# Performance work log

Hardware: AMD Instinct MI355X
Metric: run time of the kernel (lower is better)

The kernel has to match this reference:

```python
import jax, jax.numpy as jnp
import numpy as np

N_NODES = 100000
N_EDGES = 1600000
N_FEAT = 128
N_HID = 128


def cheb_conv_k2(x, edge_index, W0, W1, b):
    """PyG ChebConv with K=2, sym norm, lambda_max=2.0.
    Reduces to: out = x @ W0 + (L_hat x) @ W1 + b, where
    L_hat = 2L/lambda_max - I = -D^{-1/2} A D^{-1/2} (diagonal cancels).
    """
    n = x.shape[0]
    row, col = edge_index[0], edge_index[1]
    deg = jax.ops.segment_sum(jnp.ones_like(row, dtype=x.dtype), row, num_segments=n)
    dinv = jnp.where(deg > 0, jax.lax.rsqrt(jnp.maximum(deg, 1.0)), 0.0)
    w = -(dinv[row] * dinv[col])                     # [E] edge weights of L_hat
    tx1 = jax.ops.segment_sum(x[col] * w[:, None], row, num_segments=n)  # [N, F]
    return x @ W0 + tx1 @ W1 + b


def setup_inputs() -> dict:
    key = jax.random.key(0)
    ks = jax.random.split(key, 8)
    glorot = lambda k, fi, fo: jax.random.normal(k, (fi, fo), dtype=jnp.float32) * np.float32(np.sqrt(2.0 / (fi + fo)))
    x = jax.random.normal(ks[0], (N_NODES, N_FEAT), dtype=jnp.float32)
    edge_index = jax.random.randint(ks[1], (2, N_EDGES), 0, N_NODES, dtype=jnp.int64 if jax.config.jax_enable_x64 else jnp.int32)
    return {
        "x": x,
        "edge_index": edge_index,
        "W0_1": glorot(ks[2], N_FEAT, N_HID),
        "W1_1": glorot(ks[3], N_FEAT, N_HID),
        "b1": jnp.zeros((N_HID,), dtype=jnp.float32),
        "W0_2": glorot(ks[4], N_HID, N_HID),
        "W1_2": glorot(ks[5], N_HID, N_HID),
        "b2": jnp.zeros((N_HID,), dtype=jnp.float32),
    }


def reference(x, edge_index, W0_1, W1_1, b1, W0_2, W1_2, b2):
    # eval mode: input Dropout, dropout_adj(p=0.8), and per-layer Dropout are identity
    x1 = jax.nn.relu(cheb_conv_k2(x, edge_index, W0_1, W1_1, b1))
    x2 = jax.nn.relu(cheb_conv_k2(x1, edge_index, W0_2, W1_2, b2))
    # mean of the two layer outputs; outAct is identity
    return (x1 + x2) * 0.5
```

## Files before the change

kernel.cpp:

```cpp
#include <hip/hip_runtime.h>

#define NN 100000
#define NE 1600000
#define NF 128
#define NSTRIP2 (NN / 32)
#define NBUCK ((NN + 127) / 128)
#define CAP 2560
#define CHUNK 8192

typedef __attribute__((ext_vector_type(8))) short short8;
typedef __attribute__((ext_vector_type(4))) float f32x4;

__device__ __forceinline__ unsigned short f2b(float f) {
    union { float f; unsigned int u; } v; v.f = f;
    unsigned int u = v.u;
    unsigned int r = (u + 0x7fffu + ((u >> 16) & 1u)) >> 16;
    return (unsigned short)r;
}
__device__ __forceinline__ unsigned int cvtpk(float lo, float hi) {
    unsigned int r;
    asm("v_cvt_pk_bf16_f32 %0, %1, %2" : "=v"(r) : "v"(lo), "v"(hi));
    return r;
}

__global__ __launch_bounds__(512) void k_bin(const int* __restrict__ row,
                                             const int* __restrict__ col,
                                             int* __restrict__ gcur,
                                             unsigned int* __restrict__ gslab) {
    __shared__ int hist[NBUCK];
    __shared__ int start[NBUCK];
    __shared__ int gbase[NBUCK];
    __shared__ int scanbuf[512];
    __shared__ unsigned int stage[CHUNK];
    __shared__ unsigned short sb[CHUNK];

    const int t = threadIdx.x;
    const int e0 = blockIdx.x * CHUNK;
    const int cnt = min(CHUNK, NE - e0);

    for (int i = t; i < NBUCK; i += 512) hist[i] = 0;
    __syncthreads();
    for (int i = t; i < cnt; i += 512) atomicAdd(&hist[row[e0 + i] >> 7], 1);
    __syncthreads();

    const int b0 = t * 2;
    int s = 0;
#pragma unroll
    for (int k = 0; k < 2; ++k) { int idx = b0 + k; if (idx < NBUCK) s += hist[idx]; }
    scanbuf[t] = s;
    __syncthreads();
    for (int off = 1; off < 512; off <<= 1) {
        int u = t >= off ? scanbuf[t - off] : 0;
        __syncthreads();
        scanbuf[t] += u;
        __syncthreads();
    }
    int run = t > 0 ? scanbuf[t - 1] : 0;
#pragma unroll
    for (int k = 0; k < 2; ++k) {
        int idx = b0 + k;
        if (idx < NBUCK) { start[idx] = run; run += hist[idx]; }
    }
    __syncthreads();

    for (int i = t; i < NBUCK; i += 512) {
        int c = hist[i];
        gbase[i] = c > 0 ? atomicAdd(&gcur[i], c) : 0;
        hist[i] = start[i];
    }
    __syncthreads();

    for (int i = t; i < cnt; i += 512) {
        int r = row[e0 + i];
        int b = r >> 7;
        int p = atomicAdd(&hist[b], 1);
        stage[p] = (unsigned int)col[e0 + i] | ((unsigned int)(r & 127) << 17);
        sb[p] = (unsigned short)b;
    }
    __syncthreads();

    for (int i = t; i < cnt; i += 512) {
        int b = sb[i];
        gslab[gbase[b] + (i - start[b])] = stage[i];
    }
}

__global__ __launch_bounds__(256) void k_csr(const unsigned int* __restrict__ gslab,
                                             const int* __restrict__ gcur,
                                             int* __restrict__ offs,
                                             int* __restrict__ ccol,
                                             float* __restrict__ dinv) {
    __shared__ int rh[128];
    __shared__ int rcur[128];
    __shared__ unsigned int scol[CAP];
    __shared__ int redbuf[256];

    const int b = blockIdx.x;
    const int segbase = b * CAP;
    const int cnt = gcur[b] - segbase;
    const int t = threadIdx.x;

    int partial = 0;
    for (int i = t; i < b; i += 256) partial += gcur[i] - i * CAP;
    redbuf[t] = partial;
    if (t < 128) rh[t] = 0;
    __syncthreads();
    for (int off = 128; off > 0; off >>= 1) {
        if (t < off) redbuf[t] += redbuf[t + off];
        __syncthreads();
    }
    const int csr0 = redbuf[0];

    for (int i = t; i < cnt; i += 256) atomicAdd(&rh[gslab[segbase + i] >> 17], 1);
    __syncthreads();
    if (t == 0) {
        int run = 0;
        for (int r = 0; r < 128; ++r) { rcur[r] = run; run += rh[r]; }
    }
    __syncthreads();

    const int rbase = b * 128;
    if (t < 128 && rbase + t < NN) {
        offs[rbase + t] = csr0 + rcur[t];
        int d = rh[t];
        dinv[rbase + t] = d > 0 ? rsqrtf((float)d) : 0.0f;
    }
    if (b == NBUCK - 1 && t == 0) offs[NN] = NE;
    __syncthreads();

    for (int i = t; i < cnt; i += 256) {
        unsigned int v = gslab[segbase + i];
        int p = atomicAdd(&rcur[v >> 17], 1);
        scol[p] = v & 0x1ffff;
    }
    __syncthreads();
    for (int i = t; i < cnt; i += 256) ccol[csr0 + i] = scol[i];
}

__global__ __launch_bounds__(256) void k_quant(const float* __restrict__ x,
                                               const float* __restrict__ dinv,
                                               unsigned short* __restrict__ xq,
                                               float* __restrict__ dsc,
                                               float* __restrict__ sx) {
    int r = (blockIdx.x * 256 + threadIdx.x) >> 6;
    int lane = threadIdx.x & 63;
    float2 v = ((const float2*)x)[r * 64 + lane];
    float m = fmaxf(fabsf(v.x), fabsf(v.y));
#pragma unroll
    for (int mask = 32; mask; mask >>= 1) m = fmaxf(m, __shfl_xor(m, mask));
    float s = m * (1.0f / 127.0f);
    float inv = m > 0.0f ? 127.0f / m : 0.0f;
    int qx = (int)rintf(v.x * inv) + 128;
    int qy = (int)rintf(v.y * inv) + 128;
    xq[r * 64 + lane] = (unsigned short)(qx | (qy << 8));
    if (lane == 0) dsc[r] = dinv[r] * s;
    if (lane == 1) sx[r] = dinv[r] != 0.0f || true ? s : s;
    if (r == 0 && lane == 2) dsc[NN] = 0.0f;
}

__global__ __launch_bounds__(256) void k_pack(const float* __restrict__ W01,
                                              const float* __restrict__ W11,
                                              const float* __restrict__ W02,
                                              const float* __restrict__ W12,
                                              unsigned short* __restrict__ WP,
                                              int* __restrict__ gcur) {
    int idx = blockIdx.x * 256 + threadIdx.x;
    if (idx < NBUCK) gcur[idx] = idx * CAP;
    int mi = idx >> 14;
    int e = idx & 16383;
    const float* W = mi == 0 ? W01 : mi == 1 ? W02 : mi == 2 ? W11 : W12;
    int midx = mi == 0 ? 0 : mi == 1 ? 2 : mi == 2 ? 1 : 3;
    int k = e >> 7, n = e & 127;
    int kt = k >> 5, g = (k >> 3) & 3, j = k & 7;
    WP[midx * 16384 + (((kt * 4 + g) * 128 + n) << 3) + j] = f2b(W[e]);
}

__global__ __launch_bounds__(256) void k_gather(const int* __restrict__ offs,
                                                const int* __restrict__ ccol,
                                                const float* __restrict__ dsc,
                                                const float* __restrict__ dinv,
                                                const uint2* __restrict__ xq64,
                                                uint4* __restrict__ txb4,
                                                float qbias) {
    int r = (blockIdx.x * 256 + threadIdx.x) >> 6;
    if (r >= NN) return;
    int lane = threadIdx.x & 63;
    int fl = lane & 15, q = lane >> 4;
    int beg = offs[r], end = offs[r + 1];
    float a0 = 0.f, a1 = 0.f, a2 = 0.f, a3 = 0.f;
    float a4 = 0.f, a5 = 0.f, a6 = 0.f, a7 = 0.f, S = 0.f;
    int j = beg + q;
    for (; j + 12 < end; j += 16) {
        int c0 = ccol[j], c1 = ccol[j + 4], c2 = ccol[j + 8], c3 = ccol[j + 12];
        float w0 = dsc[c0], w1 = dsc[c1], w2 = dsc[c2], w3 = dsc[c3];
        uint2 u0 = xq64[c0 * 16 + fl];
        uint2 u1 = xq64[c1 * 16 + fl];
        uint2 u2 = xq64[c2 * 16 + fl];
        uint2 u3 = xq64[c3 * 16 + fl];
        a0 += w0 * (float)(u0.x & 0xffu)         + w1 * (float)(u1.x & 0xffu)
            + w2 * (float)(u2.x & 0xffu)         + w3 * (float)(u3.x & 0xffu);
        a1 += w0 * (float)((u0.x >> 8) & 0xffu)  + w1 * (float)((u1.x >> 8) & 0xffu)
            + w2 * (float)((u2.x >> 8) & 0xffu)  + w3 * (float)((u3.x >> 8) & 0xffu);
        a2 += w0 * (float)((u0.x >> 16) & 0xffu) + w1 * (float)((u1.x >> 16) & 0xffu)
            + w2 * (float)((u2.x >> 16) & 0xffu) + w3 * (float)((u3.x >> 16) & 0xffu);
        a3 += w0 * (float)(u0.x >> 24)           + w1 * (float)(u1.x >> 24)
            + w2 * (float)(u2.x >> 24)           + w3 * (float)(u3.x >> 24);
        a4 += w0 * (float)(u0.y & 0xffu)         + w1 * (float)(u1.y & 0xffu)
            + w2 * (float)(u2.y & 0xffu)         + w3 * (float)(u3.y & 0xffu);
        a5 += w0 * (float)((u0.y >> 8) & 0xffu)  + w1 * (float)((u1.y >> 8) & 0xffu)
            + w2 * (float)((u2.y >> 8) & 0xffu)  + w3 * (float)((u3.y >> 8) & 0xffu);
        a6 += w0 * (float)((u0.y >> 16) & 0xffu) + w1 * (float)((u1.y >> 16) & 0xffu)
            + w2 * (float)((u2.y >> 16) & 0xffu) + w3 * (float)((u3.y >> 16) & 0xffu);
        a7 += w0 * (float)(u0.y >> 24)           + w1 * (float)(u1.y >> 24)
            + w2 * (float)(u2.y >> 24)           + w3 * (float)(u3.y >> 24);
        S += w0 + w1 + w2 + w3;
    }
    if (j < end) {
        int c0 = ccol[j];
        int c1 = j + 4 < end ? ccol[j + 4] : NN;
        int c2 = j + 8 < end ? ccol[j + 8] : NN;
        float w0 = dsc[c0], w1 = dsc[c1], w2 = dsc[c2];
        uint2 u0 = xq64[c0 * 16 + fl];
        uint2 u1 = xq64[c1 * 16 + fl];
        uint2 u2 = xq64[c2 * 16 + fl];
        a0 += w0 * (float)(u0.x & 0xffu)         + w1 * (float)(u1.x & 0xffu)
            + w2 * (float)(u2.x & 0xffu);
        a1 += w0 * (float)((u0.x >> 8) & 0xffu)  + w1 * (float)((u1.x >> 8) & 0xffu)
            + w2 * (float)((u2.x >> 8) & 0xffu);
        a2 += w0 * (float)((u0.x >> 16) & 0xffu) + w1 * (float)((u1.x >> 16) & 0xffu)
            + w2 * (float)((u2.x >> 16) & 0xffu);
        a3 += w0 * (float)(u0.x >> 24)           + w1 * (float)(u1.x >> 24)
            + w2 * (float)(u2.x >> 24);
        a4 += w0 * (float)(u0.y & 0xffu)         + w1 * (float)(u1.y & 0xffu)
            + w2 * (float)(u2.y & 0xffu);
        a5 += w0 * (float)((u0.y >> 8) & 0xffu)  + w1 * (float)((u1.y >> 8) & 0xffu)
            + w2 * (float)((u2.y >> 8) & 0xffu);
        a6 += w0 * (float)((u0.y >> 16) & 0xffu) + w1 * (float)((u1.y >> 16) & 0xffu)
            + w2 * (float)((u2.y >> 16) & 0xffu);
        a7 += w0 * (float)(u0.y >> 24)           + w1 * (float)(u1.y >> 24)
            + w2 * (float)(u2.y >> 24);
        S += w0 + w1 + w2;
    }
#pragma unroll
    for (int mask = 32; mask >= 16; mask >>= 1) {
        a0 += __shfl_xor(a0, mask); a1 += __shfl_xor(a1, mask);
        a2 += __shfl_xor(a2, mask); a3 += __shfl_xor(a3, mask);
        a4 += __shfl_xor(a4, mask); a5 += __shfl_xor(a5, mask);
        a6 += __shfl_xor(a6, mask); a7 += __shfl_xor(a7, mask);
        S  += __shfl_xor(S, mask);
    }
    if (q == 0) {
        float s = -dinv[r];
        float qb = qbias * S;
        a0 = s * (a0 - qb); a1 = s * (a1 - qb); a2 = s * (a2 - qb); a3 = s * (a3 - qb);
        a4 = s * (a4 - qb); a5 = s * (a5 - qb); a6 = s * (a6 - qb); a7 = s * (a7 - qb);
        uint4 o;
        o.x = cvtpk(a0, a1);
        o.y = cvtpk(a2, a3);
        o.z = cvtpk(a4, a5);
        o.w = cvtpk(a6, a7);
        txb4[r * 16 + fl] = o;
    }
}

__global__ __launch_bounds__(256) void k_mm(const unsigned char* __restrict__ Aq,
                                            const float* __restrict__ s_in,
                                            float qoff,
                                            const unsigned short* __restrict__ Tbf,
                                            const unsigned short* __restrict__ WP0,
                                            const unsigned short* __restrict__ WP1,
                                            const float* __restrict__ bias,
                                            const float* __restrict__ dinv,
                                            float* __restrict__ out,
                                            unsigned char* __restrict__ Qout,
                                            float* __restrict__ dsc_out,
                                            float* __restrict__ s1_out,
                                            int mode) {
    __shared__ short8 Bs0[2048];
    __shared__ short8 Bs1[2048];
    {
        const short8* W0f = (const short8*)WP0;
        const short8* W1f = (const short8*)WP1;
        for (int i = threadIdx.x; i < 2048; i += 256) {
            Bs0[i] = W0f[i];
            Bs1[i] = W1f[i];
        }
    }
    __syncthreads();

    int wid = (blockIdx.x * 256 + threadIdx.x) >> 6;
    if (wid >= NSTRIP2) return;
    int lane = threadIdx.x & 63;
    int g = lane >> 4, m = lane & 15;

    short8 a[2][4], t[2][4];
#pragma unroll
    for (int s = 0; s < 2; ++s) {
        int row = wid * 32 + s * 16 + m;
        float sA = s_in[row];
        float nb = -qoff * sA;
        const unsigned char* Arow = Aq + (size_t)row * NF + g * 8;
        const short8* Tfr = (const short8*)(Tbf + (size_t)row * NF + g * 8);
#pragma unroll
        for (int kt = 0; kt < 4; ++kt) {
            uint2 u = *(const uint2*)(Arow + kt * 32);
            float f0 = fmaf((float)(u.x & 0xffu), sA, nb);
            float f1 = fmaf((float)((u.x >> 8) & 0xffu), sA, nb);
            float f2 = fmaf((float)((u.x >> 16) & 0xffu), sA, nb);
            float f3 = fmaf((float)(u.x >> 24), sA, nb);
            float f4 = fmaf((float)(u.y & 0xffu), sA, nb);
            float f5 = fmaf((float)((u.y >> 8) & 0xffu), sA, nb);
            float f6 = fmaf((float)((u.y >> 16) & 0xffu), sA, nb);
            float f7 = fmaf((float)(u.y >> 24), sA, nb);
            union { uint4 q; short8 v; } cc;
            cc.q.x = cvtpk(f0, f1);
            cc.q.y = cvtpk(f2, f3);
            cc.q.z = cvtpk(f4, f5);
            cc.q.w = cvtpk(f6, f7);
            a[s][kt] = cc.v;
            t[s][kt] = Tfr[kt * 4];
        }
    }

    const int bbase = g * 128 + m;

    f32x4 acc[2][8];
#pragma unroll
    for (int nt = 0; nt < 8; ++nt) {
        float b = bias[nt * 16 + m];
#pragma unroll
        for (int s = 0; s < 2; ++s) {
            acc[s][nt][0] = b; acc[s][nt][1] = b; acc[s][nt][2] = b; acc[s][nt][3] = b;
        }
    }

#pragma unroll
    for (int nt = 0; nt < 8; ++nt) {
#pragma unroll
        for (int kt = 0; kt < 4; ++kt) {
            short8 b0 = Bs0[bbase + kt * 512 + nt * 16];
            short8 b1 = Bs1[bbase + kt * 512 + nt * 16];
#pragma unroll
            for (int s = 0; s < 2; ++s) {
                acc[s][nt] = __builtin_amdgcn_mfma_f32_16x16x32_bf16(a[s][kt], b0, acc[s][nt], 0, 0, 0);
                acc[s][nt] = __builtin_amdgcn_mfma_f32_16x16x32_bf16(t[s][kt], b1, acc[s][nt], 0, 0, 0);
            }
        }
    }

#pragma unroll
    for (int s = 0; s < 2; ++s)
#pragma unroll
        for (int nt = 0; nt < 8; ++nt)
#pragma unroll
            for (int r = 0; r < 4; ++r) acc[s][nt][r] = fmaxf(acc[s][nt][r], 0.0f);

    if (mode == 0) {
#pragma unroll
        for (int s = 0; s < 2; ++s) {
            int rbase = wid * 32 + s * 16 + g * 4;
            float mr[4] = {0.0f, 0.0f, 0.0f, 0.0f};
#pragma unroll
            for (int nt = 0; nt < 8; ++nt)
#pragma unroll
                for (int r = 0; r < 4; ++r) mr[r] = fmaxf(mr[r], acc[s][nt][r]);
#pragma unroll
            for (int mask = 1; mask < 16; mask <<= 1)
#pragma unroll
                for (int r = 0; r < 4; ++r) mr[r] = fmaxf(mr[r], __shfl_xor(mr[r], mask));

            float inv[4], s1v[4];
#pragma unroll
            for (int r = 0; r < 4; ++r) {
                s1v[r] = mr[r] * (1.0f / 255.0f);
                inv[r] = mr[r] > 0.0f ? 255.0f / mr[r] : 0.0f;
            }
#pragma unroll
            for (int nt = 0; nt < 8; ++nt) {
                int c = nt * 16 + m;
#pragma unroll
                for (int r = 0; r < 4; ++r) {
                    int qv = (int)rintf(acc[s][nt][r] * inv[r]);
                    qv = qv > 255 ? 255 : qv;
                    Qout[(size_t)(rbase + r) * NF + c] = (unsigned char)qv;
                }
            }
            if (m == 0) {
#pragma unroll
                for (int r = 0; r < 4; ++r) {
                    s1_out[rbase + r] = s1v[r];
                    dsc_out[rbase + r] = dinv[rbase + r] * s1v[r];
                }
            }
        }
    } else {
#pragma unroll
        for (int s = 0; s < 2; ++s) {
            int rbase = wid * 32 + s * 16 + g * 4;
            float sR[4];
#pragma unroll
            for (int r = 0; r < 4; ++r) sR[r] = s_in[rbase + r];
#pragma unroll
            for (int nt = 0; nt < 8; ++nt) {
                int c = nt * 16 + m;
#pragma unroll
                for (int r = 0; r < 4; ++r) {
                    size_t o = (size_t)(rbase + r) * NF + c;
                    float x1v = sR[r] * (float)Aq[o];
                    out[o] = 0.5f * (x1v + acc[s][nt][r]);
                }
            }
        }
    }
}

extern "C" void kernel_launch(void* const* d_in, const int* in_sizes, int n_in,
                              void* d_out, int out_size, void* d_ws, size_t ws_size,
                              hipStream_t stream) {
    const float* x   = (const float*)d_in[0];
    const int*   ei  = (const int*)d_in[1];
    const float* W01 = (const float*)d_in[2];
    const float* W11 = (const float*)d_in[3];
    const float* b1  = (const float*)d_in[4];
    const float* W02 = (const float*)d_in[5];
    const float* W12 = (const float*)d_in[6];
    const float* b2  = (const float*)d_in[7];
    float* out = (float*)d_out;

    const int* row = ei;
    const int* col = ei + NE;

    char* ws = (char*)d_ws;
    int*            gcur  = (int*)(ws);
    float*          dinv  = (float*)(ws + 6400);
    int*            offs  = (int*)(ws + 406400);
    int*            ccol  = (int*)(ws + 806416);
    unsigned short* WP    = (unsigned short*)(ws + 7206416);
    float*          dsc   = (float*)(ws + 7337488);
    float*          s1a   = (float*)(ws + 7737504);
    float*          sx    = (float*)(ws + 8137504);
    unsigned short* xq    = (unsigned short*)(ws + 8537504);
    unsigned int*   txb   = (unsigned int*)(ws + 21337632);
    unsigned int*   gslab = (unsigned int*)(ws + 21337632);

    unsigned char*  xq8 = (unsigned char*)xq;
    unsigned short* WP01 = WP;
    unsigned short* WP11 = WP + 16384;
    unsigned short* WP02 = WP + 32768;
    unsigned short* WP12 = WP + 49152;

    k_pack <<<(4 * 16384) / 256, 256, 0, stream>>>(W01, W11, W02, W12, WP, gcur);
    k_bin  <<<(NE + CHUNK - 1) / CHUNK, 512, 0, stream>>>(row, col, gcur, gslab);
    k_csr  <<<NBUCK, 256, 0, stream>>>(gslab, gcur, offs, ccol, dinv);

    k_quant<<<(NN * 64) / 256, 256, 0, stream>>>(x, dinv, xq, dsc, sx);

    const int gatherBlocks = (NN * 64) / 256;
    const int mmBlocks = (NSTRIP2 * 64 + 255) / 256;

    k_gather<<<gatherBlocks, 256, 0, stream>>>(offs, ccol, dsc, dinv,
                                               (const uint2*)xq, (uint4*)txb, 128.0f);
    k_mm    <<<mmBlocks, 256, 0, stream>>>(xq8, sx, 128.0f, (const unsigned short*)txb,
                                           WP01, WP11, b1, dinv, out, xq8, dsc, s1a, 0);

    k_gather<<<gatherBlocks, 256, 0, stream>>>(offs, ccol, dsc, dinv,
                                               (const uint2*)xq, (uint4*)txb, 0.0f);
    k_mm    <<<mmBlocks, 256, 0, stream>>>(xq8, s1a, 0.0f, (const unsigned short*)txb,
                                           WP02, WP12, b2, dinv, out, xq8, dsc, s1a, 1);
}
```

Baseline: 207.2 us.

## Slice quantized features into eight 16-byte slabs and gather per slice

Stores the int8-quantized node features as eight separate slabs of 16 bytes per node instead of one contiguous 128-byte row. The gather kernel now runs one block per (16 rows, slice) pair with 1024 threads, four lanes per edge reading 4 bytes each, and writes its bf16 output into the matching slice. The matmul kernel's loads and its requantized output are updated to the new slab layout. The intent is a smaller per-slice working set for the random neighbour reads, which could improve cache reuse. In exchange, the edge indices and weights are re-read once per slice, each edge access is a 16-byte fragment rather than a full row, and adjacent blocks touch different slices, so locality may not improve.

```diff
diff --git a/kernel.cpp b/kernel.cpp
--- a/kernel.cpp
+++ b/kernel.cpp
@@ -7,6 +7,7 @@
 #define NBUCK ((NN + 127) / 128)
 #define CAP 2560
 #define CHUNK 8192
+#define SLAB ((size_t)(NN + 1) * 16)
 
 typedef __attribute__((ext_vector_type(8))) short short8;
 typedef __attribute__((ext_vector_type(4))) float f32x4;
@@ -139,7 +140,7 @@
 
 __global__ __launch_bounds__(256) void k_quant(const float* __restrict__ x,
                                                const float* __restrict__ dinv,
-                                               unsigned short* __restrict__ xq,
+                                               unsigned char* __restrict__ xq8,
                                                float* __restrict__ dsc,
                                                float* __restrict__ sx) {
     int r = (blockIdx.x * 256 + threadIdx.x) >> 6;
@@ -152,9 +153,10 @@
     float inv = m > 0.0f ? 127.0f / m : 0.0f;
     int qx = (int)rintf(v.x * inv) + 128;
     int qy = (int)rintf(v.y * inv) + 128;
-    xq[r * 64 + lane] = (unsigned short)(qx | (qy << 8));
+    *(unsigned short*)(xq8 + (size_t)(lane >> 3) * SLAB + (size_t)r * 16 + ((2 * lane) & 15))
+        = (unsigned short)(qx | (qy << 8));
     if (lane == 0) dsc[r] = dinv[r] * s;
-    if (lane == 1) sx[r] = dinv[r] != 0.0f || true ? s : s;
+    if (lane == 1) sx[r] = s;
     if (r == 0 && lane == 2) dsc[NN] = 0.0f;
 }
 
@@ -175,91 +177,47 @@
     WP[midx * 16384 + (((kt * 4 + g) * 128 + n) << 3) + j] = f2b(W[e]);
 }
 
-__global__ __launch_bounds__(256) void k_gather(const int* __restrict__ offs,
-                                                const int* __restrict__ ccol,
-                                                const float* __restrict__ dsc,
-                                                const float* __restrict__ dinv,
-                                                const uint2* __restrict__ xq64,
-                                                uint4* __restrict__ txb4,
-                                                float qbias) {
-    int r = (blockIdx.x * 256 + threadIdx.x) >> 6;
+__global__ __launch_bounds__(1024) void k_gather(const int* __restrict__ offs,
+                                                 const int* __restrict__ ccol,
+                                                 const float* __restrict__ dsc,
+                                                 const float* __restrict__ dinv,
+                                                 const unsigned char* __restrict__ xq8,
+                                                 uint2* __restrict__ txb2,
+                                                 float qbias) {
+    const int slice = blockIdx.x & 7;
+    const int r = (blockIdx.x >> 3) * 16 + (threadIdx.x >> 6);
     if (r >= NN) return;
-    int lane = threadIdx.x & 63;
-    int fl = lane & 15, q = lane >> 4;
+    const int lane = threadIdx.x & 63;
+    const int eg = lane >> 2, fq = lane & 3;
+    const unsigned* xs = (const unsigned*)(xq8 + (size_t)slice * SLAB);
     int beg = offs[r], end = offs[r + 1];
-    float a0 = 0.f, a1 = 0.f, a2 = 0.f, a3 = 0.f;
-    float a4 = 0.f, a5 = 0.f, a6 = 0.f, a7 = 0.f, S = 0.f;
-    int j = beg + q;
-    for (; j + 12 < end; j += 16) {
-        int c0 = ccol[j], c1 = ccol[j + 4], c2 = ccol[j + 8], c3 = ccol[j + 12];
-        float w0 = dsc[c0], w1 = dsc[c1], w2 = dsc[c2], w3 = dsc[c3];
-        uint2 u0 = xq64[c0 * 16 + fl];
-        uint2 u1 = xq64[c1 * 16 + fl];
-        uint2 u2 = xq64[c2 * 16 + fl];
-        uint2 u3 = xq64[c3 * 16 + fl];
-        a0 += w0 * (float)(u0.x & 0xffu)         + w1 * (float)(u1.x & 0xffu)
-            + w2 * (float)(u2.x & 0xffu)         + w3 * (float)(u3.x & 0xffu);
-        a1 += w0 * (float)((u0.x >> 8) & 0xffu)  + w1 * (float)((u1.x >> 8) & 0xffu)
-            + w2 * (float)((u2.x >> 8) & 0xffu)  + w3 * (float)((u3.x >> 8) & 0xffu);
-        a2 += w0 * (float)((u0.x >> 16) & 0xffu) + w1 * (float)((u1.x >> 16) & 0xffu)
-            + w2 * (float)((u2.x >> 16) & 0xffu) + w3 * (float)((u3.x >> 16) & 0xffu);
-        a3 += w0 * (float)(u0.x >> 24)           + w1 * (float)(u1.x >> 24)
-            + w2 * (float)(u2.x >> 24)           + w3 * (float)(u3.x >> 24);
-        a4 += w0 * (float)(u0.y & 0xffu)         + w1 * (float)(u1.y & 0xffu)
-            + w2 * (float)(u2.y & 0xffu)         + w3 * (float)(u3.y & 0xffu);
-        a5 += w0 * (float)((u0.y >> 8) & 0xffu)  + w1 * (float)((u1.y >> 8) & 0xffu)
-            + w2 * (float)((u2.y >> 8) & 0xffu)  + w3 * (float)((u3.y >> 8) & 0xffu);
-        a6 += w0 * (float)((u0.y >> 16) & 0xffu) + w1 * (float)((u1.y >> 16) & 0xffu)
-            + w2 * (float)((u2.y >> 16) & 0xffu) + w3 * (float)((u3.y >> 16) & 0xffu);
-        a7 += w0 * (float)(u0.y >> 24)           + w1 * (float)(u1.y >> 24)
-            + w2 * (float)(u2.y >> 24)           + w3 * (float)(u3.y >> 24);
-        S += w0 + w1 + w2 + w3;
-    }
-    if (j < end) {
-        int c0 = ccol[j];
-        int c1 = j + 4 < end ? ccol[j + 4] : NN;
-        int c2 = j + 8 < end ? ccol[j + 8] : NN;
-        float w0 = dsc[c0], w1 = dsc[c1], w2 = dsc[c2];
-        uint2 u0 = xq64[c0 * 16 + fl];
-        uint2 u1 = xq64[c1 * 16 + fl];
-        uint2 u2 = xq64[c2 * 16 + fl];
-        a0 += w0 * (float)(u0.x & 0xffu)         + w1 * (float)(u1.x & 0xffu)
-            + w2 * (float)(u2.x & 0xffu);
-        a1 += w0 * (float)((u0.x >> 8) & 0xffu)  + w1 * (float)((u1.x >> 8) & 0xffu)
-            + w2 * (float)((u2.x >> 8) & 0xffu);
-        a2 += w0 * (float)((u0.x >> 16) & 0xffu) + w1 * (float)((u1.x >> 16) & 0xffu)
-            + w2 * (float)((u2.x >> 16) & 0xffu);
-        a3 += w0 * (float)(u0.x >> 24)           + w1 * (float)(u1.x >> 24)
-            + w2 * (float)(u2.x >> 24);
-        a4 += w0 * (float)(u0.y & 0xffu)         + w1 * (float)(u1.y & 0xffu)
-            + w2 * (float)(u2.y & 0xffu);
-        a5 += w0 * (float)((u0.y >> 8) & 0xffu)  + w1 * (float)((u1.y >> 8) & 0xffu)
-            + w2 * (float)((u2.y >> 8) & 0xffu);
-        a6 += w0 * (float)((u0.y >> 16) & 0xffu) + w1 * (float)((u1.y >> 16) & 0xffu)
-            + w2 * (float)((u2.y >> 16) & 0xffu);
-        a7 += w0 * (float)(u0.y >> 24)           + w1 * (float)(u1.y >> 24)
-            + w2 * (float)(u2.y >> 24);
-        S += w0 + w1 + w2;
-    }
-#pragma unroll
-    for (int mask = 32; mask >= 16; mask >>= 1) {
+    float a0 = 0.f, a1 = 0.f, a2 = 0.f, a3 = 0.f, S = 0.f;
+    int niter = (end - beg + 15) >> 4;
+    for (int it = 0; it < niter; ++it) {
+        int j = beg + eg + it * 16;
+        int c = j < end ? ccol[j] : NN;
+        float w = dsc[c];
+        unsigned u = xs[c * 4 + fq];
+        a0 += w * (float)(u & 0xffu);
+        a1 += w * (float)((u >> 8) & 0xffu);
+        a2 += w * (float)((u >> 16) & 0xffu);
+        a3 += w * (float)(u >> 24);
+        S += w;
+    }
+#pragma unroll
+    for (int mask = 4; mask <= 32; mask <<= 1) {
         a0 += __shfl_xor(a0, mask); a1 += __shfl_xor(a1, mask);
         a2 += __shfl_xor(a2, mask); a3 += __shfl_xor(a3, mask);
-        a4 += __shfl_xor(a4, mask); a5 += __shfl_xor(a5, mask);
-        a6 += __shfl_xor(a6, mask); a7 += __shfl_xor(a7, mask);
         S  += __shfl_xor(S, mask);
     }
-    if (q == 0) {
+    if (eg == 0) {
         float s = -dinv[r];
         float qb = qbias * S;
         a0 = s * (a0 - qb); a1 = s * (a1 - qb); a2 = s * (a2 - qb); a3 = s * (a3 - qb);
-        a4 = s * (a4 - qb); a5 = s * (a5 - qb); a6 = s * (a6 - qb); a7 = s * (a7 - qb);
-        uint4 o;
+        uint2 o;
         o.x = cvtpk(a0, a1);
         o.y = cvtpk(a2, a3);
-        o.z = cvtpk(a4, a5);
-        o.w = cvtpk(a6, a7);
-        txb4[r * 16 + fl] = o;
+        txb2[(size_t)r * 32 + slice * 4 + fq] = o;
     }
 }
 
@@ -299,11 +257,11 @@
         int row = wid * 32 + s * 16 + m;
         float sA = s_in[row];
         float nb = -qoff * sA;
-        const unsigned char* Arow = Aq + (size_t)row * NF + g * 8;
         const short8* Tfr = (const short8*)(Tbf + (size_t)row * NF + g * 8);
 #pragma unroll
         for (int kt = 0; kt < 4; ++kt) {
-            uint2 u = *(const uint2*)(Arow + kt * 32);
+            uint2 u = *(const uint2*)(Aq + (size_t)(kt * 2 + (g >> 1)) * SLAB
+                                         + (size_t)row * 16 + (g & 1) * 8);
             float f0 = fmaf((float)(u.x & 0xffu), sA, nb);
             float f1 = fmaf((float)((u.x >> 8) & 0xffu), sA, nb);
             float f2 = fmaf((float)((u.x >> 16) & 0xffu), sA, nb);
@@ -382,7 +340,7 @@
                 for (int r = 0; r < 4; ++r) {
                     int qv = (int)rintf(acc[s][nt][r] * inv[r]);
                     qv = qv > 255 ? 255 : qv;
-                    Qout[(size_t)(rbase + r) * NF + c] = (unsigned char)qv;
+                    Qout[(size_t)nt * SLAB + (size_t)(rbase + r) * 16 + m] = (unsigned char)qv;
                 }
             }
             if (m == 0) {
@@ -406,7 +364,7 @@
 #pragma unroll
                 for (int r = 0; r < 4; ++r) {
                     size_t o = (size_t)(rbase + r) * NF + c;
-                    float x1v = sR[r] * (float)Aq[o];
+                    float x1v = sR[r] * (float)Aq[(size_t)nt * SLAB + (size_t)(rbase + r) * 16 + m];
                     out[o] = 0.5f * (x1v + acc[s][nt][r]);
                 }
             }
@@ -439,11 +397,10 @@
     float*          dsc   = (float*)(ws + 7337488);
     float*          s1a   = (float*)(ws + 7737504);
     float*          sx    = (float*)(ws + 8137504);
-    unsigned short* xq    = (unsigned short*)(ws + 8537504);
+    unsigned char*  xq8   = (unsigned char*)(ws + 8537504);
     unsigned int*   txb   = (unsigned int*)(ws + 21337632);
     unsigned int*   gslab = (unsigned int*)(ws + 21337632);
 
-    unsigned char*  xq8 = (unsigned char*)xq;
     unsigned short* WP01 = WP;
     unsigned short* WP11 = WP + 16384;
     unsigned short* WP02 = WP + 32768;
@@ -453,18 +410,18 @@
     k_bin  <<<(NE + CHUNK - 1) / CHUNK, 512, 0, stream>>>(row, col, gcur, gslab);
     k_csr  <<<NBUCK, 256, 0, stream>>>(gslab, gcur, offs, ccol, dinv);
 
-    k_quant<<<(NN * 64) / 256, 256, 0, stream>>>(x, dinv, xq, dsc, sx);
-
-    const int gatherBlocks = (NN * 64) / 256;
+    k_quant<<<(NN * 64) / 256, 256, 0, stream>>>(x, dinv, xq8, dsc, sx);
+
+    const int gatherBlocks = ((NN + 15) / 16) * 8;
     const int mmBlocks = (NSTRIP2 * 64 + 255) / 256;
 
-    k_gather<<<gatherBlocks, 256, 0, stream>>>(offs, ccol, dsc, dinv,
-                                               (const uint2*)xq, (uint4*)txb, 128.0f);
+    k_gather<<<gatherBlocks, 1024, 0, stream>>>(offs, ccol, dsc, dinv,
+                                                xq8, (uint2*)txb, 128.0f);
     k_mm    <<<mmBlocks, 256, 0, stream>>>(xq8, sx, 128.0f, (const unsigned short*)txb,
                                            WP01, WP11, b1, dinv, out, xq8, dsc, s1a, 0);
 
-    k_gather<<<gatherBlocks, 256, 0, stream>>>(offs, ccol, dsc, dinv,
-                                               (const uint2*)xq, (uint4*)txb, 0.0f);
+    k_gather<<<gatherBlocks, 1024, 0, stream>>>(offs, ccol, dsc, dinv,
+                                                xq8, (uint2*)txb, 0.0f);
     k_mm    <<<mmBlocks, 256, 0, stream>>>(xq8, s1a, 0.0f, (const unsigned short*)txb,
                                            WP02, WP12, b2, dinv, out, xq8, dsc, s1a, 1);
 }
```

Measured after the change: 533.4 us. 2.57x slower.
